# Kernel optimization log

Measured on AMD Instinct MI355X. Metric: run time of the kernel, lower is better.

Reference implementation:

```python
import jax, jax.numpy as jnp
import numpy as np

B = 65536      # batch of (state, action) pairs
DIM_S = 64     # input feature dim
DIM_C = 8      # number of options / experts
H = 256        # hidden width (two hidden layers)


def setup_inputs() -> dict:
    key = jax.random.key(0)
    ks = jax.random.split(key, 7)
    s = 0.05  # small init scale
    st = jax.random.normal(ks[0], (B, DIM_S), dtype=jnp.float32)
    # Batched expert weights: one slice per expert (dim_c experts).
    W1 = jax.random.normal(ks[1], (DIM_C, DIM_S, H), dtype=jnp.float32) * s
    b1 = jax.random.normal(ks[2], (DIM_C, H), dtype=jnp.float32) * s
    W2 = jax.random.normal(ks[3], (DIM_C, H, H), dtype=jnp.float32) * s
    b2 = jax.random.normal(ks[4], (DIM_C, H), dtype=jnp.float32) * s
    W3 = jax.random.normal(ks[5], (DIM_C, H, 1), dtype=jnp.float32) * s
    b3 = jax.random.normal(ks[6], (DIM_C, 1), dtype=jnp.float32) * s
    return {"st": st, "W1": W1, "b1": b1, "W2": W2, "b2": b2,
            "W3": W3, "b3": b3}


def reference(st, W1, b1, W2, b2, W3, b3):
    # Equivalent of torch.stack([m(st) for m in self.discriminator], dim=1):
    # every expert MLP (dim_s -> H -> H -> 1, ReLU) applied to the same st,
    # expressed as batched GEMMs over the expert axis c.
    h = jax.nn.relu(jnp.einsum('bs,csh->bch', st, W1) + b1[None])   # [B, C, H]
    h = jax.nn.relu(jnp.einsum('bch,chk->bck', h, W2) + b2[None])   # [B, C, H]
    d = jnp.einsum('bch,cho->bco', h, W3) + b3[None]                # [B, C, 1]
    return d
```

## Files before the change

### kernel.cpp

```cpp
#include <hip/hip_runtime.h>
#include <hip/hip_bf16.h>

typedef __bf16 bf16x8 __attribute__((ext_vector_type(8)));
typedef float  f32x4  __attribute__((ext_vector_type(4)));

static constexpr int S  = 64;
static constexpr int C  = 8;
static constexpr int HD = 256;

__device__ __forceinline__ unsigned short f2bf(float f) {
  __hip_bfloat16 b = __float2bfloat16(f);
  unsigned short u;
  __builtin_memcpy(&u, &b, 2);
  return u;
}

__device__ __forceinline__ void gl2lds16(const void* g, void* l) {
  __builtin_amdgcn_global_load_lds(
      (const __attribute__((address_space(1))) unsigned int*)g,
      (__attribute__((address_space(3))) unsigned int*)l, 16, 0, 0);
}

__global__ __launch_bounds__(256) void prep_weights(
    const float* __restrict__ W1, const float* __restrict__ W2,
    unsigned short* __restrict__ W1T, unsigned short* __restrict__ W2T)
{
  __shared__ float tile[32][33];
  const int tid = threadIdx.x, cl = tid & 31, r0 = tid >> 5;
  const int b = blockIdx.x;
  if (b < 512) {
    const int c = b >> 6, t = b & 63, kt = t >> 3, nt = t & 7;
    const float* src = W2 + c * 65536;
    #pragma unroll
    for (int i = 0; i < 4; ++i) {
      int r = r0 + 8 * i;
      tile[r][cl] = src[(kt * 32 + r) * 256 + nt * 32 + cl];
    }
    __syncthreads();
    unsigned short* dst = W2T + c * 65536;
    #pragma unroll
    for (int i = 0; i < 4; ++i) {
      int r = r0 + 8 * i;
      dst[(nt * 32 + r) * 256 + kt * 32 + cl] = f2bf(tile[cl][r]);
    }
  } else {
    const int bb = b - 512;
    const int c = bb >> 4, t = bb & 15, st2 = t >> 3, ht = t & 7;
    const float* src = W1 + c * 16384;
    #pragma unroll
    for (int i = 0; i < 4; ++i) {
      int r = r0 + 8 * i;
      tile[r][cl] = src[(st2 * 32 + r) * 256 + ht * 32 + cl];
    }
    __syncthreads();
    unsigned short* dst = W1T + c * 16384;
    #pragma unroll
    for (int i = 0; i < 4; ++i) {
      int r = r0 + 8 * i;
      dst[(ht * 32 + r) * 64 + st2 * 32 + cl] = f2bf(tile[cl][r]);
    }
  }
}

__global__ __launch_bounds__(256, 2) void moe_fused(
    const float* __restrict__ st,
    const unsigned short* __restrict__ W1T,
    const unsigned short* __restrict__ W2T,
    const float* __restrict__ b1,
    const float* __restrict__ b2,
    const float* __restrict__ W3,
    const float* __restrict__ b3,
    float* __restrict__ out)
{
  constexpr int LDT = 72;

  __shared__ __align__(16) unsigned short sT[256 * LDT];
  __shared__ __align__(16) unsigned short sU[2 * 32 * 256];

  const int tid  = threadIdx.x;
  const int lane = tid & 63;
  const int wv   = tid >> 6;
  const int l15  = lane & 15;
  const int q    = lane >> 4;
  const int c    = blockIdx.x >> 8;
  const int row0 = (blockIdx.x & 255) * 256;

  const unsigned short* W1c = W1T + c * HD * S;
  const unsigned short* W2c = W2T + c * HD * HD;

  {
    #pragma unroll
    for (int it = 0; it < 8; ++it) {
      const int r = wv * 64 + it * 8 + (lane >> 3);
      const int g = lane & 7;
      const float4* p = reinterpret_cast<const float4*>(
          st + (size_t)(row0 + r) * S + g * 8);
      float4 x = p[0], y = p[1];
      union { uint4 u4; unsigned u[4]; } pk;
      __asm__("v_cvt_pk_bf16_f32 %0, %1, %2" : "=v"(pk.u[0]) : "v"(x.x), "v"(x.y));
      __asm__("v_cvt_pk_bf16_f32 %0, %1, %2" : "=v"(pk.u[1]) : "v"(x.z), "v"(x.w));
      __asm__("v_cvt_pk_bf16_f32 %0, %1, %2" : "=v"(pk.u[2]) : "v"(y.x), "v"(y.y));
      __asm__("v_cvt_pk_bf16_f32 %0, %1, %2" : "=v"(pk.u[3]) : "v"(y.z), "v"(y.w));
      *reinterpret_cast<uint4*>(sU + r * 64 + ((g ^ (r & 7)) << 3)) = pk.u4;
    }
  }
  __asm__ __volatile__("s_waitcnt lgkmcnt(0)" ::: "memory");

  bf16x8 aF[4][4][2];
  #pragma unroll
  for (int cc = 0; cc < 4; ++cc) {
    f32x4 bias[4];
    #pragma unroll
    for (int mt = 0; mt < 4; ++mt)
      bias[mt] = *reinterpret_cast<const f32x4*>(
          b1 + c * HD + cc * 64 + mt * 16 + q * 4);

    f32x4 acc[4][4];
    #pragma unroll
    for (int mt = 0; mt < 4; ++mt)
      #pragma unroll
      for (int nt = 0; nt < 4; ++nt)
        acc[mt][nt] = bias[mt];

    #pragma unroll
    for (int ks = 0; ks < 2; ++ks) {
      bf16x8 aW[4];
      #pragma unroll
      for (int mt = 0; mt < 4; ++mt)
        aW[mt] = *reinterpret_cast<const bf16x8*>(
            W1c + (cc * 64 + mt * 16 + l15) * S + ks * 32 + q * 8);
      bf16x8 bB[4];
      #pragma unroll
      for (int nt = 0; nt < 4; ++nt) {
        const int r = wv * 64 + nt * 16 + l15;
        const int g = ks * 4 + q;
        bB[nt] = *reinterpret_cast<const bf16x8*>(
            sU + r * 64 + ((g ^ (r & 7)) << 3));
      }
      __builtin_amdgcn_s_setprio(1);
      #pragma unroll
      for (int mt = 0; mt < 4; ++mt)
        #pragma unroll
        for (int nt = 0; nt < 4; ++nt)
          acc[mt][nt] = __builtin_amdgcn_mfma_f32_16x16x32_bf16(
              aW[mt], bB[nt], acc[mt][nt], 0, 0, 0);
      __builtin_amdgcn_s_setprio(0);
    }

    #pragma unroll
    for (int mt = 0; mt < 4; ++mt) {
      #pragma unroll
      for (int nt = 0; nt < 4; ++nt) {
        float v0 = acc[mt][nt][0]; v0 = v0 > 0.f ? v0 : 0.f;
        float v1 = acc[mt][nt][1]; v1 = v1 > 0.f ? v1 : 0.f;
        float v2 = acc[mt][nt][2]; v2 = v2 > 0.f ? v2 : 0.f;
        float v3 = acc[mt][nt][3]; v3 = v3 > 0.f ? v3 : 0.f;
        uint2 pk;
        __asm__("v_cvt_pk_bf16_f32 %0, %1, %2" : "=v"(pk.x) : "v"(v0), "v"(v1));
        __asm__("v_cvt_pk_bf16_f32 %0, %1, %2" : "=v"(pk.y) : "v"(v2), "v"(v3));
        *reinterpret_cast<uint2*>(
            sT + (wv * 64 + nt * 16 + l15) * LDT + mt * 16 + q * 4) = pk;
      }
    }
    __asm__ __volatile__("s_waitcnt lgkmcnt(0)" ::: "memory");
    #pragma unroll
    for (int rt = 0; rt < 4; ++rt)
      #pragma unroll
      for (int k2 = 0; k2 < 2; ++k2)
        aF[cc][rt][k2] = *reinterpret_cast<const bf16x8*>(
            sT + (wv * 64 + rt * 16 + l15) * LDT + k2 * 32 + q * 8);
    __asm__ __volatile__("s_waitcnt lgkmcnt(0)" ::: "memory");
  }

  float pb2v[8][2], pw3v[8][2];
  #pragma unroll
  for (int ch = 0; ch < 8; ++ch)
    #pragma unroll
    for (int ct = 0; ct < 2; ++ct) {
      const int n = ch * 32 + ct * 16 + l15;
      pb2v[ch][ct] = b2[c * HD + n];
      pw3v[ch][ct] = W3[c * HD + n];
    }
  const float bb3 = b3[c];

  __syncthreads();

  #pragma unroll
  for (int pc = 0; pc < 2; ++pc) {
    unsigned short* buf = sU + pc * (32 * 256);
    #pragma unroll
    for (int i = 0; i < 4; ++i) {
      const int b2i = wv * 4 + i;
      const int r   = b2i * 2 + (lane >> 5);
      const int j   = (lane & 31) ^ (r & 7);
      gl2lds16(W2c + (pc * 32 + r) * 256 + j * 8, buf + b2i * 512);
    }
  }
  __syncthreads();

  float dacc[4][4];
  #pragma unroll
  for (int rt = 0; rt < 4; ++rt)
    #pragma unroll
    for (int r = 0; r < 4; ++r) dacc[rt][r] = 0.f;

  #pragma unroll
  for (int ch = 0; ch < 8; ++ch) {
    const unsigned short* buf = sU + (ch & 1) * (32 * 256);

    f32x4 acc[4][2];
    #pragma unroll
    for (int rt = 0; rt < 4; ++rt)
      #pragma unroll
      for (int ct = 0; ct < 2; ++ct) {
        const float bv = pb2v[ch][ct];
        acc[rt][ct] = (f32x4){bv, bv, bv, bv};
      }

    #pragma unroll
    for (int ks = 0; ks < 8; ++ks) {
      const int jj = ks * 4 + q;
      const int cc = ks >> 1, k2 = ks & 1;
      #pragma unroll
      for (int ct = 0; ct < 2; ++ct) {
        const int nl = ct * 16 + l15;
        bf16x8 b = *reinterpret_cast<const bf16x8*>(
            buf + nl * 256 + ((jj ^ (l15 & 7)) << 3));
        __builtin_amdgcn_s_setprio(1);
        #pragma unroll
        for (int rt = 0; rt < 4; ++rt)
          acc[rt][ct] = __builtin_amdgcn_mfma_f32_16x16x32_bf16(
              aF[cc][rt][k2], b, acc[rt][ct], 0, 0, 0);
        __builtin_amdgcn_s_setprio(0);
      }
    }

    #pragma unroll
    for (int ct = 0; ct < 2; ++ct) {
      const float w3v = pw3v[ch][ct];
      #pragma unroll
      for (int rt = 0; rt < 4; ++rt)
        #pragma unroll
        for (int r = 0; r < 4; ++r) {
          float v = acc[rt][ct][r];
          v = v > 0.f ? v : 0.f;
          dacc[rt][r] += v * w3v;
        }
    }

    __syncthreads();
    if (ch < 6) {
      unsigned short* nbuf = sU + (ch & 1) * (32 * 256);
      #pragma unroll
      for (int i = 0; i < 4; ++i) {
        const int b2i = wv * 4 + i;
        const int r   = b2i * 2 + (lane >> 5);
        const int j   = (lane & 31) ^ (r & 7);
        gl2lds16(W2c + ((ch + 2) * 32 + r) * 256 + j * 8, nbuf + b2i * 512);
      }
    }
  }

  #pragma unroll
  for (int rt = 0; rt < 4; ++rt)
    #pragma unroll
    for (int r = 0; r < 4; ++r) {
      float v = dacc[rt][r];
      v += __shfl_xor(v, 1);
      v += __shfl_xor(v, 2);
      v += __shfl_xor(v, 4);
      v += __shfl_xor(v, 8);
      dacc[rt][r] = v;
    }

  if (l15 == 0) {
    const int rbase = row0 + wv * 64 + q * 4;
    #pragma unroll
    for (int rt = 0; rt < 4; ++rt)
      #pragma unroll
      for (int r = 0; r < 4; ++r)
        out[(rbase + rt * 16 + r) * C + c] = dacc[rt][r] + bb3;
  }
}

extern "C" void kernel_launch(void* const* d_in, const int* in_sizes, int n_in,
                              void* d_out, int out_size, void* d_ws, size_t ws_size,
                              hipStream_t stream)
{
  const float* st = (const float*)d_in[0];
  const float* W1 = (const float*)d_in[1];
  const float* b1 = (const float*)d_in[2];
  const float* W2 = (const float*)d_in[3];
  const float* b2 = (const float*)d_in[4];
  const float* W3 = (const float*)d_in[5];
  const float* b3 = (const float*)d_in[6];
  float* out = (float*)d_out;

  unsigned short* W1T = (unsigned short*)d_ws;
  unsigned short* W2T = W1T + C * HD * S;

  prep_weights<<<dim3(640), dim3(256), 0, stream>>>(W1, W2, W1T, W2T);
  moe_fused<<<dim3(2048), dim3(256), 0, stream>>>(st, W1T, W2T, b1, b2, W3, b3, out);
}
```

Baseline: 164.9 us.

## Switch both GEMM layers to 32x32x16 MFMA and load st directly to registers

Both layers now use 32x32x16 bf16 MFMA tiles instead of 16x16x32, which cuts the number of LDS fragment reads per MFMA and the number of MFMA issues. The st input is loaded straight into B-operand registers instead of being staged through LDS. The first W2 chunk prefetch now starts before layer 1, so it overlaps with that computation. The cost is a different accumulator layout, a longer shuffle reduction over 32 lanes, and possibly more register pressure from the 16-wide accumulators.

Result: slower. 176.1 us (+6.7%).

```diff
diff --git a/kernel.cpp b/kernel.cpp
--- a/kernel.cpp
+++ b/kernel.cpp
@@ -3,6 +3,7 @@
 
 typedef __bf16 bf16x8 __attribute__((ext_vector_type(8)));
 typedef float  f32x4  __attribute__((ext_vector_type(4)));
+typedef float  f32x16 __attribute__((ext_vector_type(16)));
 
 static constexpr int S  = 64;
 static constexpr int C  = 8;
@@ -80,172 +81,141 @@
   const int tid  = threadIdx.x;
   const int lane = tid & 63;
   const int wv   = tid >> 6;
-  const int l15  = lane & 15;
-  const int q    = lane >> 4;
+  const int l31  = lane & 31;
+  const int h5   = lane >> 5;
   const int c    = blockIdx.x >> 8;
   const int row0 = (blockIdx.x & 255) * 256;
+  const int wrow = row0 + wv * 64;
 
   const unsigned short* W1c = W1T + c * HD * S;
   const unsigned short* W2c = W2T + c * HD * HD;
 
-  {
-    #pragma unroll
-    for (int it = 0; it < 8; ++it) {
-      const int r = wv * 64 + it * 8 + (lane >> 3);
-      const int g = lane & 7;
-      const float4* p = reinterpret_cast<const float4*>(
-          st + (size_t)(row0 + r) * S + g * 8);
-      float4 x = p[0], y = p[1];
-      union { uint4 u4; unsigned u[4]; } pk;
+  #pragma unroll
+  for (int pc = 0; pc < 2; ++pc) {
+    unsigned short* buf = sU + pc * (32 * 256);
+    #pragma unroll
+    for (int i = 0; i < 4; ++i) {
+      const int b2i = wv * 4 + i;
+      const int r   = b2i * 2 + (lane >> 5);
+      const int j   = (lane & 31) ^ (r & 7);
+      gl2lds16(W2c + (pc * 32 + r) * 256 + j * 8, buf + b2i * 512);
+    }
+  }
+
+  float b2v[8], w3v[8];
+  #pragma unroll
+  for (int ch = 0; ch < 8; ++ch) {
+    b2v[ch] = b2[c * HD + ch * 32 + l31];
+    w3v[ch] = W3[c * HD + ch * 32 + l31];
+  }
+  const float bb3 = b3[c];
+
+  bf16x8 bB[4][2];
+  #pragma unroll
+  for (int nt = 0; nt < 2; ++nt)
+    #pragma unroll
+    for (int ks = 0; ks < 4; ++ks) {
+      const float* rp = st + (size_t)(wrow + nt * 32 + l31) * S + ks * 16 + h5 * 8;
+      float4 x = *reinterpret_cast<const float4*>(rp);
+      float4 y = *reinterpret_cast<const float4*>(rp + 4);
+      union { bf16x8 v; unsigned u[4]; } pk;
       __asm__("v_cvt_pk_bf16_f32 %0, %1, %2" : "=v"(pk.u[0]) : "v"(x.x), "v"(x.y));
       __asm__("v_cvt_pk_bf16_f32 %0, %1, %2" : "=v"(pk.u[1]) : "v"(x.z), "v"(x.w));
       __asm__("v_cvt_pk_bf16_f32 %0, %1, %2" : "=v"(pk.u[2]) : "v"(y.x), "v"(y.y));
       __asm__("v_cvt_pk_bf16_f32 %0, %1, %2" : "=v"(pk.u[3]) : "v"(y.z), "v"(y.w));
-      *reinterpret_cast<uint4*>(sU + r * 64 + ((g ^ (r & 7)) << 3)) = pk.u4;
-    }
-  }
-  __asm__ __volatile__("s_waitcnt lgkmcnt(0)" ::: "memory");
-
-  bf16x8 aF[4][4][2];
-  #pragma unroll
-  for (int cc = 0; cc < 4; ++cc) {
-    f32x4 bias[4];
-    #pragma unroll
-    for (int mt = 0; mt < 4; ++mt)
-      bias[mt] = *reinterpret_cast<const f32x4*>(
-          b1 + c * HD + cc * 64 + mt * 16 + q * 4);
-
-    f32x4 acc[4][4];
-    #pragma unroll
-    for (int mt = 0; mt < 4; ++mt)
-      #pragma unroll
-      for (int nt = 0; nt < 4; ++nt)
-        acc[mt][nt] = bias[mt];
-
-    #pragma unroll
-    for (int ks = 0; ks < 2; ++ks) {
+      bB[ks][nt] = pk.v;
+    }
+
+  bf16x8 aF[2][16];
+  #pragma unroll
+  for (int grp = 0; grp < 4; ++grp) {
+    #pragma unroll
+    for (int mt2 = 0; mt2 < 2; ++mt2) {
+      const int mt = grp * 2 + mt2;
       bf16x8 aW[4];
       #pragma unroll
-      for (int mt = 0; mt < 4; ++mt)
-        aW[mt] = *reinterpret_cast<const bf16x8*>(
-            W1c + (cc * 64 + mt * 16 + l15) * S + ks * 32 + q * 8);
-      bf16x8 bB[4];
-      #pragma unroll
-      for (int nt = 0; nt < 4; ++nt) {
-        const int r = wv * 64 + nt * 16 + l15;
-        const int g = ks * 4 + q;
-        bB[nt] = *reinterpret_cast<const bf16x8*>(
-            sU + r * 64 + ((g ^ (r & 7)) << 3));
-      }
+      for (int ks = 0; ks < 4; ++ks)
+        aW[ks] = *reinterpret_cast<const bf16x8*>(
+            W1c + (size_t)(mt * 32 + l31) * S + ks * 16 + h5 * 8);
+
+      union { f32x4 q[4]; f32x16 v; } bu;
+      #pragma unroll
+      for (int g = 0; g < 4; ++g)
+        bu.q[g] = *reinterpret_cast<const f32x4*>(
+            b1 + c * HD + mt * 32 + 8 * g + 4 * h5);
+
       __builtin_amdgcn_s_setprio(1);
-      #pragma unroll
-      for (int mt = 0; mt < 4; ++mt)
+      f32x16 acc0 = __builtin_amdgcn_mfma_f32_32x32x16_bf16(aW[0], bB[0][0], bu.v, 0, 0, 0);
+      f32x16 acc1 = __builtin_amdgcn_mfma_f32_32x32x16_bf16(aW[0], bB[0][1], bu.v, 0, 0, 0);
+      #pragma unroll
+      for (int ks = 1; ks < 4; ++ks) {
+        acc0 = __builtin_amdgcn_mfma_f32_32x32x16_bf16(aW[ks], bB[ks][0], acc0, 0, 0, 0);
+        acc1 = __builtin_amdgcn_mfma_f32_32x32x16_bf16(aW[ks], bB[ks][1], acc1, 0, 0, 0);
+      }
+      __builtin_amdgcn_s_setprio(0);
+
+      #pragma unroll
+      for (int nt = 0; nt < 2; ++nt) {
+        const f32x16& A = nt ? acc1 : acc0;
+        const int rbase = (wv * 64 + nt * 32 + l31) * LDT + mt2 * 32;
         #pragma unroll
-        for (int nt = 0; nt < 4; ++nt)
-          acc[mt][nt] = __builtin_amdgcn_mfma_f32_16x16x32_bf16(
-              aW[mt], bB[nt], acc[mt][nt], 0, 0, 0);
-      __builtin_amdgcn_s_setprio(0);
-    }
-
-    #pragma unroll
-    for (int mt = 0; mt < 4; ++mt) {
-      #pragma unroll
-      for (int nt = 0; nt < 4; ++nt) {
-        float v0 = acc[mt][nt][0]; v0 = v0 > 0.f ? v0 : 0.f;
-        float v1 = acc[mt][nt][1]; v1 = v1 > 0.f ? v1 : 0.f;
-        float v2 = acc[mt][nt][2]; v2 = v2 > 0.f ? v2 : 0.f;
-        float v3 = acc[mt][nt][3]; v3 = v3 > 0.f ? v3 : 0.f;
-        uint2 pk;
-        __asm__("v_cvt_pk_bf16_f32 %0, %1, %2" : "=v"(pk.x) : "v"(v0), "v"(v1));
-        __asm__("v_cvt_pk_bf16_f32 %0, %1, %2" : "=v"(pk.y) : "v"(v2), "v"(v3));
-        *reinterpret_cast<uint2*>(
-            sT + (wv * 64 + nt * 16 + l15) * LDT + mt * 16 + q * 4) = pk;
+        for (int g = 0; g < 4; ++g) {
+          float v0 = A[4*g+0]; v0 = v0 > 0.f ? v0 : 0.f;
+          float v1 = A[4*g+1]; v1 = v1 > 0.f ? v1 : 0.f;
+          float v2 = A[4*g+2]; v2 = v2 > 0.f ? v2 : 0.f;
+          float v3 = A[4*g+3]; v3 = v3 > 0.f ? v3 : 0.f;
+          uint2 pk;
+          __asm__("v_cvt_pk_bf16_f32 %0, %1, %2" : "=v"(pk.x) : "v"(v0), "v"(v1));
+          __asm__("v_cvt_pk_bf16_f32 %0, %1, %2" : "=v"(pk.y) : "v"(v2), "v"(v3));
+          *reinterpret_cast<uint2*>(sT + rbase + 8 * g + 4 * h5) = pk;
+        }
       }
     }
     __asm__ __volatile__("s_waitcnt lgkmcnt(0)" ::: "memory");
     #pragma unroll
-    for (int rt = 0; rt < 4; ++rt)
-      #pragma unroll
-      for (int k2 = 0; k2 < 2; ++k2)
-        aF[cc][rt][k2] = *reinterpret_cast<const bf16x8*>(
-            sT + (wv * 64 + rt * 16 + l15) * LDT + k2 * 32 + q * 8);
+    for (int rt = 0; rt < 2; ++rt)
+      #pragma unroll
+      for (int s2 = 0; s2 < 4; ++s2)
+        aF[rt][grp * 4 + s2] = *reinterpret_cast<const bf16x8*>(
+            sT + (wv * 64 + rt * 32 + l31) * LDT + s2 * 16 + h5 * 8);
     __asm__ __volatile__("s_waitcnt lgkmcnt(0)" ::: "memory");
   }
 
-  float pb2v[8][2], pw3v[8][2];
-  #pragma unroll
-  for (int ch = 0; ch < 8; ++ch)
-    #pragma unroll
-    for (int ct = 0; ct < 2; ++ct) {
-      const int n = ch * 32 + ct * 16 + l15;
-      pb2v[ch][ct] = b2[c * HD + n];
-      pw3v[ch][ct] = W3[c * HD + n];
-    }
-  const float bb3 = b3[c];
-
   __syncthreads();
 
-  #pragma unroll
-  for (int pc = 0; pc < 2; ++pc) {
-    unsigned short* buf = sU + pc * (32 * 256);
-    #pragma unroll
-    for (int i = 0; i < 4; ++i) {
-      const int b2i = wv * 4 + i;
-      const int r   = b2i * 2 + (lane >> 5);
-      const int j   = (lane & 31) ^ (r & 7);
-      gl2lds16(W2c + (pc * 32 + r) * 256 + j * 8, buf + b2i * 512);
-    }
-  }
-  __syncthreads();
-
-  float dacc[4][4];
-  #pragma unroll
-  for (int rt = 0; rt < 4; ++rt)
-    #pragma unroll
-    for (int r = 0; r < 4; ++r) dacc[rt][r] = 0.f;
+  float dacc0[16], dacc1[16];
+  #pragma unroll
+  for (int r = 0; r < 16; ++r) { dacc0[r] = 0.f; dacc1[r] = 0.f; }
 
   #pragma unroll
   for (int ch = 0; ch < 8; ++ch) {
     const unsigned short* buf = sU + (ch & 1) * (32 * 256);
 
-    f32x4 acc[4][2];
-    #pragma unroll
-    for (int rt = 0; rt < 4; ++rt)
-      #pragma unroll
-      for (int ct = 0; ct < 2; ++ct) {
-        const float bv = pb2v[ch][ct];
-        acc[rt][ct] = (f32x4){bv, bv, bv, bv};
-      }
-
-    #pragma unroll
-    for (int ks = 0; ks < 8; ++ks) {
-      const int jj = ks * 4 + q;
-      const int cc = ks >> 1, k2 = ks & 1;
-      #pragma unroll
-      for (int ct = 0; ct < 2; ++ct) {
-        const int nl = ct * 16 + l15;
-        bf16x8 b = *reinterpret_cast<const bf16x8*>(
-            buf + nl * 256 + ((jj ^ (l15 & 7)) << 3));
-        __builtin_amdgcn_s_setprio(1);
-        #pragma unroll
-        for (int rt = 0; rt < 4; ++rt)
-          acc[rt][ct] = __builtin_amdgcn_mfma_f32_16x16x32_bf16(
-              aF[cc][rt][k2], b, acc[rt][ct], 0, 0, 0);
-        __builtin_amdgcn_s_setprio(0);
-      }
-    }
-
-    #pragma unroll
-    for (int ct = 0; ct < 2; ++ct) {
-      const float w3v = pw3v[ch][ct];
-      #pragma unroll
-      for (int rt = 0; rt < 4; ++rt)
-        #pragma unroll
-        for (int r = 0; r < 4; ++r) {
-          float v = acc[rt][ct][r];
-          v = v > 0.f ? v : 0.f;
-          dacc[rt][r] += v * w3v;
-        }
+    f32x16 b2i;
+    #pragma unroll
+    for (int r = 0; r < 16; ++r) b2i[r] = b2v[ch];
+
+    f32x16 acc0, acc1;
+    #pragma unroll
+    for (int stp = 0; stp < 16; ++stp) {
+      const int j = stp * 2 + h5;
+      bf16x8 bF = *reinterpret_cast<const bf16x8*>(
+          buf + l31 * 256 + ((j ^ (l31 & 7)) << 3));
+      __builtin_amdgcn_s_setprio(1);
+      if (stp == 0) {
+        acc0 = __builtin_amdgcn_mfma_f32_32x32x16_bf16(aF[0][0], bF, b2i, 0, 0, 0);
+        acc1 = __builtin_amdgcn_mfma_f32_32x32x16_bf16(aF[1][0], bF, b2i, 0, 0, 0);
+      } else {
+        acc0 = __builtin_amdgcn_mfma_f32_32x32x16_bf16(aF[0][stp], bF, acc0, 0, 0, 0);
+        acc1 = __builtin_amdgcn_mfma_f32_32x32x16_bf16(aF[1][stp], bF, acc1, 0, 0, 0);
+      }
+      __builtin_amdgcn_s_setprio(0);
+    }
+
+    #pragma unroll
+    for (int r = 0; r < 16; ++r) {
+      float v0 = acc0[r]; v0 = v0 > 0.f ? v0 : 0.f; dacc0[r] += v0 * w3v[ch];
+      float v1 = acc1[r]; v1 = v1 > 0.f ? v1 : 0.f; dacc1[r] += v1 * w3v[ch];
     }
 
     __syncthreads();
@@ -253,33 +223,32 @@
       unsigned short* nbuf = sU + (ch & 1) * (32 * 256);
       #pragma unroll
       for (int i = 0; i < 4; ++i) {
-        const int b2i = wv * 4 + i;
-        const int r   = b2i * 2 + (lane >> 5);
-        const int j   = (lane & 31) ^ (r & 7);
-        gl2lds16(W2c + ((ch + 2) * 32 + r) * 256 + j * 8, nbuf + b2i * 512);
-      }
-    }
-  }
-
-  #pragma unroll
-  for (int rt = 0; rt < 4; ++rt)
-    #pragma unroll
-    for (int r = 0; r < 4; ++r) {
-      float v = dacc[rt][r];
-      v += __shfl_xor(v, 1);
-      v += __shfl_xor(v, 2);
-      v += __shfl_xor(v, 4);
-      v += __shfl_xor(v, 8);
-      dacc[rt][r] = v;
-    }
-
-  if (l15 == 0) {
-    const int rbase = row0 + wv * 64 + q * 4;
-    #pragma unroll
-    for (int rt = 0; rt < 4; ++rt)
-      #pragma unroll
-      for (int r = 0; r < 4; ++r)
-        out[(rbase + rt * 16 + r) * C + c] = dacc[rt][r] + bb3;
+        const int b2i2 = wv * 4 + i;
+        const int r    = b2i2 * 2 + (lane >> 5);
+        const int j    = (lane & 31) ^ (r & 7);
+        gl2lds16(W2c + ((ch + 2) * 32 + r) * 256 + j * 8, nbuf + b2i2 * 512);
+      }
+    }
+  }
+
+  #pragma unroll
+  for (int r = 0; r < 16; ++r) {
+    float v0 = dacc0[r], v1 = dacc1[r];
+    v0 += __shfl_xor(v0, 1);  v1 += __shfl_xor(v1, 1);
+    v0 += __shfl_xor(v0, 2);  v1 += __shfl_xor(v1, 2);
+    v0 += __shfl_xor(v0, 4);  v1 += __shfl_xor(v1, 4);
+    v0 += __shfl_xor(v0, 8);  v1 += __shfl_xor(v1, 8);
+    v0 += __shfl_xor(v0, 16); v1 += __shfl_xor(v1, 16);
+    dacc0[r] = v0; dacc1[r] = v1;
+  }
+
+  if (l31 == 0) {
+    #pragma unroll
+    for (int r = 0; r < 16; ++r) {
+      const int rr = (r & 3) + 8 * (r >> 2) + 4 * h5;
+      out[(size_t)(wrow + rr) * C + c]      = dacc0[r] + bb3;
+      out[(size_t)(wrow + 32 + rr) * C + c] = dacc1[r] + bb3;
+    }
   }
 }
 
```

## Load st fragments directly to registers and prefetch W2 during layer one

Applied to the files above, without the earlier changes.

Each wave now loads its st rows straight into registers in MFMA fragment layout and converts them to bf16, so the LDS staging of st and its lgkmcnt wait go away. Since sU is no longer needed for st, the async global-to-LDS load of the first two W2 chunks is issued at kernel start and overlaps with the layer-one compute, which also removes one __syncthreads. In exchange the kernel holds more registers (the raw float4 and bf16 fragments), which may lower occupancy, and the st global reads are less coalesced.

Measured after the change: 172.3 us. 1.04x slower.

```diff
diff --git a/kernel.cpp b/kernel.cpp
--- a/kernel.cpp
+++ b/kernel.cpp
@@ -84,27 +84,46 @@
   const int q    = lane >> 4;
   const int c    = blockIdx.x >> 8;
   const int row0 = (blockIdx.x & 255) * 256;
+  const int wrow = row0 + wv * 64;
 
   const unsigned short* W1c = W1T + c * HD * S;
   const unsigned short* W2c = W2T + c * HD * HD;
 
-  {
-    #pragma unroll
-    for (int it = 0; it < 8; ++it) {
-      const int r = wv * 64 + it * 8 + (lane >> 3);
-      const int g = lane & 7;
-      const float4* p = reinterpret_cast<const float4*>(
-          st + (size_t)(row0 + r) * S + g * 8);
-      float4 x = p[0], y = p[1];
-      union { uint4 u4; unsigned u[4]; } pk;
+  float4 sraw[8][2];
+  #pragma unroll
+  for (int nt = 0; nt < 4; ++nt)
+    #pragma unroll
+    for (int ks = 0; ks < 2; ++ks) {
+      const float* rp = st + (size_t)(wrow + nt * 16 + l15) * S + ks * 32 + q * 8;
+      sraw[ks * 4 + nt][0] = *reinterpret_cast<const float4*>(rp);
+      sraw[ks * 4 + nt][1] = *reinterpret_cast<const float4*>(rp + 4);
+    }
+
+  #pragma unroll
+  for (int pc = 0; pc < 2; ++pc) {
+    unsigned short* buf = sU + pc * (32 * 256);
+    #pragma unroll
+    for (int i = 0; i < 4; ++i) {
+      const int b2i = wv * 4 + i;
+      const int r   = b2i * 2 + (lane >> 5);
+      const int j   = (lane & 31) ^ (r & 7);
+      gl2lds16(W2c + (pc * 32 + r) * 256 + j * 8, buf + b2i * 512);
+    }
+  }
+
+  bf16x8 bB[2][4];
+  #pragma unroll
+  for (int nt = 0; nt < 4; ++nt)
+    #pragma unroll
+    for (int ks = 0; ks < 2; ++ks) {
+      float4 x = sraw[ks * 4 + nt][0], y = sraw[ks * 4 + nt][1];
+      union { bf16x8 v; unsigned u[4]; } pk;
       __asm__("v_cvt_pk_bf16_f32 %0, %1, %2" : "=v"(pk.u[0]) : "v"(x.x), "v"(x.y));
       __asm__("v_cvt_pk_bf16_f32 %0, %1, %2" : "=v"(pk.u[1]) : "v"(x.z), "v"(x.w));
       __asm__("v_cvt_pk_bf16_f32 %0, %1, %2" : "=v"(pk.u[2]) : "v"(y.x), "v"(y.y));
       __asm__("v_cvt_pk_bf16_f32 %0, %1, %2" : "=v"(pk.u[3]) : "v"(y.z), "v"(y.w));
-      *reinterpret_cast<uint4*>(sU + r * 64 + ((g ^ (r & 7)) << 3)) = pk.u4;
-    }
-  }
-  __asm__ __volatile__("s_waitcnt lgkmcnt(0)" ::: "memory");
+      bB[ks][nt] = pk.v;
+    }
 
   bf16x8 aF[4][4][2];
   #pragma unroll
@@ -129,21 +148,13 @@
       for (int mt = 0; mt < 4; ++mt)
         aW[mt] = *reinterpret_cast<const bf16x8*>(
             W1c + (cc * 64 + mt * 16 + l15) * S + ks * 32 + q * 8);
-      bf16x8 bB[4];
-      #pragma unroll
-      for (int nt = 0; nt < 4; ++nt) {
-        const int r = wv * 64 + nt * 16 + l15;
-        const int g = ks * 4 + q;
-        bB[nt] = *reinterpret_cast<const bf16x8*>(
-            sU + r * 64 + ((g ^ (r & 7)) << 3));
-      }
       __builtin_amdgcn_s_setprio(1);
       #pragma unroll
       for (int mt = 0; mt < 4; ++mt)
         #pragma unroll
         for (int nt = 0; nt < 4; ++nt)
           acc[mt][nt] = __builtin_amdgcn_mfma_f32_16x16x32_bf16(
-              aW[mt], bB[nt], acc[mt][nt], 0, 0, 0);
+              aW[mt], bB[ks][nt], acc[mt][nt], 0, 0, 0);
       __builtin_amdgcn_s_setprio(0);
     }
 
@@ -183,19 +194,6 @@
     }
   const float bb3 = b3[c];
 
-  __syncthreads();
-
-  #pragma unroll
-  for (int pc = 0; pc < 2; ++pc) {
-    unsigned short* buf = sU + pc * (32 * 256);
-    #pragma unroll
-    for (int i = 0; i < 4; ++i) {
-      const int b2i = wv * 4 + i;
-      const int r   = b2i * 2 + (lane >> 5);
-      const int j   = (lane & 31) ^ (r & 7);
-      gl2lds16(W2c + (pc * 32 + r) * 256 + j * 8, buf + b2i * 512);
-    }
-  }
   __syncthreads();
 
   float dacc[4][4];
```
